# Kernel tuning notes

Hardware: AMD Instinct MI355X
Metric: run time of the kernel (lower is better)

## Reference

```python
import jax, jax.numpy as jnp
import numpy as np
import math

DIM = 256
PATCH = 16  # Patchnum
H = W = 64  # feature_size
B = 16


def _conv(x, w, pad):
    # x: [B,C,H,W], w: [O,I,kh,kw]
    return jax.lax.conv_general_dilated(
        x, w, window_strides=(1, 1), padding=[(pad, pad), (pad, pad)],
        dimension_numbers=('NCHW', 'OIHW', 'NCHW'))


def setup_inputs() -> dict:
    key = jax.random.key(0)
    ks = jax.random.split(key, 6)
    fan = DIM * 9
    s3 = 1.0 / math.sqrt(fan)
    s1 = 1.0 / math.sqrt(DIM)
    return {
        'e': jax.random.normal(ks[0], (B, DIM, H, W), dtype=jnp.float32),
        'pam_out': jax.random.normal(ks[1], (B, DIM, PATCH, PATCH), dtype=jnp.float32),
        'q_w': jax.random.uniform(ks[2], (DIM, DIM, 3, 3), jnp.float32, -s3, s3),
        'k_w': jax.random.uniform(ks[3], (DIM, DIM, 3, 3), jnp.float32, -s3, s3),
        'v_w': jax.random.uniform(ks[4], (DIM, DIM, 3, 3), jnp.float32, -s3, s3),
        'proj_w': jax.random.uniform(ks[5], (DIM, DIM, 1, 1), jnp.float32, -s1, s1),
    }


def reference(e, pam_out, q_w, k_w, v_w, proj_w):
    b, c, h, w = e.shape
    # AdaptiveAvgPool2d((PATCH, PATCH)) with h % PATCH == 0 -> mean pooling
    fh, fw = h // PATCH, w // PATCH
    max_e = e.reshape(b, c, PATCH, fh, PATCH, fw).mean(axis=(3, 5))
    q = _conv(max_e, q_w, 1).reshape(b, c, PATCH * PATCH)      # [b,c,P^2]
    k = _conv(pam_out, k_w, 1).reshape(b, c, PATCH * PATCH)    # [b,c,P^2]
    v = _conv(e, v_w, 1).reshape(b, c, h * w)                  # [b,c,HW]
    # L2 normalize along token dim (torch F.normalize, eps=1e-12)
    q = q / jnp.maximum(jnp.linalg.norm(q, axis=-1, keepdims=True), 1e-12)
    k = k / jnp.maximum(jnp.linalg.norm(k, axis=-1, keepdims=True), 1e-12)
    attn = jnp.einsum('bcn,bdn->bcd', q, k) / math.sqrt(c)     # [b,c,c]
    attn = jax.nn.softmax(attn, axis=-1)
    out = jnp.einsum('bcd,bdn->bcn', attn, v).reshape(b, c, h, w)
    out = _conv(out, proj_w, 0) + e
    return out
```

## Files before the change

kernel.cpp:

```cpp
#include <hip/hip_runtime.h>
#include <hip/hip_bf16.h>

#define NB 16
#define NC 256
#define NPIX 4096

typedef __attribute__((ext_vector_type(8))) short short8;
typedef __attribute__((ext_vector_type(4))) short short4v;
typedef __attribute__((ext_vector_type(4))) float f32x4;

static __device__ __forceinline__ ushort f2bf(float f) {
    __hip_bfloat16 h = __float2bfloat16(f);
    return *(ushort*)&h;
}

static __device__ __forceinline__ void gload_lds16(const ushort* g, ushort* l) {
    __builtin_amdgcn_global_load_lds(
        (const __attribute__((address_space(1))) unsigned int*)g,
        (__attribute__((address_space(3))) unsigned int*)l, 16, 0, 0);
}

__global__ void __launch_bounds__(256) prep_k(
    const float* __restrict__ e, const float* __restrict__ pam,
    const float* __restrict__ qw, const float* __restrict__ kw,
    const float* __restrict__ vw, const float* __restrict__ pw,
    ushort* __restrict__ maxeT, ushort* __restrict__ pamT,
    ushort* __restrict__ wqT, ushort* __restrict__ wkT,
    ushort* __restrict__ pbf, ushort* __restrict__ vwT,
    float* __restrict__ qnorm, float* __restrict__ knorm) {
    __shared__ float smem[9216];
    int blk = blockIdx.x, t = threadIdx.x;
    if (blk < 1024) {
        int b = blk >> 6, c0 = (blk & 63) * 4;
        int py = t >> 4, px4 = (t & 15) * 4;
        float s[4];
#pragma unroll
        for (int cc = 0; cc < 4; ++cc) {
            const float* p = e + (size_t)(b * 256 + c0 + cc) * NPIX;
            float a = 0.f;
#pragma unroll
            for (int r = 0; r < 4; ++r) {
                float4 v = *(const float4*)(p + (py * 4 + r) * 64 + px4);
                a += v.x + v.y + v.z + v.w;
            }
            s[cc] = a * 0.0625f;
        }
        short4v v;
#pragma unroll
        for (int cc = 0; cc < 4; ++cc) v[cc] = (short)f2bf(s[cc]);
        *(short4v*)(maxeT + (size_t)b * 65536 + (size_t)t * 256 + c0) = v;
    } else if (blk < 1280) {
        int bb = blk - 1024;
        int b = bb >> 4, cg = bb & 15;
        float (*lt)[256] = (float(*)[256])smem;
#pragma unroll
        for (int cc = 0; cc < 16; ++cc)
            lt[cc][t] = pam[(size_t)(b * 256 + cg * 16 + cc) * 256 + t];
        __syncthreads();
        ushort* dstb = pamT + (size_t)b * 65536 + (size_t)t * 256 + cg * 16;
#pragma unroll
        for (int g = 0; g < 2; ++g) {
            short8 v;
#pragma unroll
            for (int k = 0; k < 8; ++k) v[k] = (short)f2bf(lt[g * 8 + k][t]);
            *(short8*)(dstb + g * 8) = v;
        }
    } else if (blk < 1792) {
        int idx = blk - 1280;
        const float* src = (idx < 256) ? qw : kw;
        ushort* dst = (idx < 256) ? wqT : wkT;
        int o = idx & 255;
        float wv[9];
#pragma unroll
        for (int j = 0; j < 9; ++j) wv[j] = src[(size_t)o * 2304 + t * 9 + j];
#pragma unroll
        for (int j = 0; j < 9; ++j) dst[(size_t)j * 65536 + (size_t)o * 256 + t] = f2bf(wv[j]);
    } else if (blk < 1808) {
        int base = (blk - 1792) * 4096;
        for (int g = 0; g < 16; ++g) {
            int idx = base + g * 256 + t;
            pbf[idx] = f2bf(pw[idx]);
        }
    } else if (blk < 1872) {
        int d0 = (blk - 1808) * 4;
        float* lt = smem;
        for (int u = 0; u < 36; ++u) lt[u * 256 + t] = vw[(size_t)d0 * 2304 + u * 256 + t];
        __syncthreads();
#pragma unroll
        for (int r = 0; r < 9; ++r) {
            int idx = r * 256 + t;
            int i = idx / 9, j = idx % 9;
            short4v v;
#pragma unroll
            for (int dd = 0; dd < 4; ++dd) v[dd] = (short)f2bf(lt[dd * 2304 + idx]);
            *(short4v*)(vwT + ((size_t)(j * 256 + i)) * 256 + d0) = v;
        }
    } else {
        for (int g = 0; g < 16; ++g) {
            qnorm[g * 256 + t] = 0.f;
            knorm[g * 256 + t] = 0.f;
        }
    }
}

__global__ void __launch_bounds__(256, 2) conv16_mfma(const ushort* __restrict__ maxeT,
                                                      const ushort* __restrict__ pamT,
                                                      const ushort* __restrict__ wqT,
                                                      const ushort* __restrict__ wkT,
                                                      ushort* __restrict__ qb,
                                                      ushort* __restrict__ kTb,
                                                      float* __restrict__ qnorm,
                                                      float* __restrict__ knorm) {
    int blk = blockIdx.x;
    int qk = blk >> 8;
    int b  = (blk >> 4) & 15;
    int og = (blk >> 2) & 3;
    int tg = blk & 3;
    const ushort* inT = qk ? pamT : maxeT;
    const ushort* wt  = qk ? wkT : wqT;
    ushort* outp      = qk ? kTb : qb;
    float* nrm        = qk ? knorm : qnorm;
    int tid = threadIdx.x, wid = tid >> 6, lane = tid & 63;
    int wm = wid >> 1, wn = wid & 1;
    int kq = lane >> 4, l16 = lane & 15;
    int ty0 = tg * 4;
    __shared__ ushort Bs[96][256];
    __shared__ ushort As[2][64][64];
    const ushort* itb = inT + (size_t)b * 65536;
    {
#pragma unroll
        for (int j = 0; j < 12; ++j) {
            int d = (j * 4 + wid) * 64 + lane;
            int tok = d >> 5, u = d & 31;
            int lr = tok >> 4, tx = tok & 15;
            int gy = min(max(ty0 - 1 + lr, 0), 15);
            gload_lds16(itb + (gy * 16 + tx) * 256 + ((u ^ (tok & 7)) * 8),
                        &Bs[0][0] + (size_t)(j * 4 + wid) * 512);
        }
    }
    int aoff[2];
#pragma unroll
    for (int j = 0; j < 2; ++j) {
        int d = (j * 4 + wid) * 64 + lane;
        int o = d >> 3, u = d & 7;
        aoff[j] = (og * 64 + o) * 256 + ((u ^ (o & 7)) * 8);
    }
    auto stageA = [&](int s, int buf) {
        const ushort* base = wt + (size_t)(s >> 2) * 65536 + (s & 3) * 64;
#pragma unroll
        for (int j = 0; j < 2; ++j)
            gload_lds16(base + aoff[j], &As[buf][0][0] + (size_t)(j * 4 + wid) * 512);
    };
    stageA(0, 0);
    stageA(1, 1);
    __syncthreads();
    f32x4 acc[2][2];
#pragma unroll
    for (int mf = 0; mf < 2; ++mf)
#pragma unroll
        for (int nf = 0; nf < 2; ++nf) acc[mf][nf] = (f32x4){0.f, 0.f, 0.f, 0.f};
    const short8 zf = {};
    for (int s = 0; s < 36; ++s) {
        int tap = s >> 2, kh = s & 3;
        int dy = tap / 3 - 1, dx = tap % 3 - 1;
        const ushort* bp[2]; bool ok[2]; int lt7[2];
#pragma unroll
        for (int nf = 0; nf < 2; ++nf) {
            int n = tg * 64 + wn * 32 + nf * 16 + l16;
            int ny = (n >> 4) + dy, nx = (n & 15) + dx;
            ok[nf] = ((unsigned)ny < 16u) && ((unsigned)nx < 16u);
            int lrc = min(max(ny - ty0 + 1, 0), 5);
            int nxc = min(max(nx, 0), 15);
            int ltok = lrc * 16 + nxc;
            bp[nf] = &Bs[ltok][0];
            lt7[nf] = ltok & 7;
        }
#pragma unroll
        for (int kc = 0; kc < 2; ++kc) {
            int ua = kc * 4 + kq;
            int ub = kh * 8 + kc * 4 + kq;
            short8 af[2], bfr[2];
#pragma unroll
            for (int mf = 0; mf < 2; ++mf) {
                int o = wm * 32 + mf * 16 + l16;
                af[mf] = *(const short8*)(&As[s & 1][o][(ua ^ (o & 7)) * 8]);
            }
#pragma unroll
            for (int nf = 0; nf < 2; ++nf) {
                short8 v = *(const short8*)(bp[nf] + ((ub ^ lt7[nf]) * 8));
                bfr[nf] = ok[nf] ? v : zf;
            }
#pragma unroll
            for (int mf = 0; mf < 2; ++mf)
#pragma unroll
                for (int nf = 0; nf < 2; ++nf)
                    acc[mf][nf] = __builtin_amdgcn_mfma_f32_16x16x32_bf16(af[mf], bfr[nf], acc[mf][nf], 0, 0, 0);
        }
        __syncthreads();
        if (s + 2 < 36) stageA(s + 2, s & 1);
    }
    float ss[2][4];
#pragma unroll
    for (int mf = 0; mf < 2; ++mf)
#pragma unroll
        for (int r = 0; r < 4; ++r) ss[mf][r] = 0.f;
#pragma unroll
    for (int mf = 0; mf < 2; ++mf)
#pragma unroll
        for (int nf = 0; nf < 2; ++nf)
#pragma unroll
            for (int r = 0; r < 4; ++r) ss[mf][r] += acc[mf][nf][r] * acc[mf][nf][r];
#pragma unroll
    for (int mf = 0; mf < 2; ++mf)
#pragma unroll
        for (int r = 0; r < 4; ++r) {
#pragma unroll
            for (int off = 1; off < 16; off <<= 1) ss[mf][r] += __shfl_xor(ss[mf][r], off, 64);
        }
    if (l16 == 0) {
#pragma unroll
        for (int mf = 0; mf < 2; ++mf)
#pragma unroll
            for (int r = 0; r < 4; ++r)
                atomicAdd(&nrm[b * 256 + og * 64 + wm * 32 + mf * 16 + kq * 4 + r], ss[mf][r]);
    }
    ushort* ob = outp + (size_t)b * 65536;
#pragma unroll
    for (int mf = 0; mf < 2; ++mf)
#pragma unroll
        for (int nf = 0; nf < 2; ++nf) {
            int col = tg * 64 + wn * 32 + nf * 16 + l16;
#pragma unroll
            for (int r = 0; r < 4; ++r) {
                int row = og * 64 + wm * 32 + mf * 16 + kq * 4 + r;
                ob[(size_t)row * 256 + col] = f2bf(acc[mf][nf][r]);
            }
        }
}

__global__ void __launch_bounds__(512) attn_mfma(const ushort* __restrict__ qb,
                                                 const ushort* __restrict__ kTb,
                                                 const float* __restrict__ qnorm,
                                                 const float* __restrict__ knorm,
                                                 ushort* __restrict__ attnT) {
    int blk = blockIdx.x;
    int b = (blk & 7) + 8 * ((blk >> 3) & 1);
    int cg = blk >> 4;
    int tid = threadIdx.x, wid = tid >> 6, lane = tid & 63;
    int rw = wid & 3, chf = wid >> 2;
    int kq = lane >> 4, l16 = lane & 15;
    int c0w = cg * 64 + rw * 16;
    int lrow = rw * 16 + kq * 4;
    f32x4 acc[8];
#pragma unroll
    for (int nf = 0; nf < 8; ++nf) acc[nf] = (f32x4){0.f, 0.f, 0.f, 0.f};
    const ushort* qp = qb + (size_t)b * 65536;
    const ushort* kp = kTb + (size_t)b * 65536 + (size_t)(chf * 128) * 256;
    for (int kc = 0; kc < 8; ++kc) {
        short8 af = *(const short8*)(qp + (size_t)(c0w + l16) * 256 + kc * 32 + kq * 8);
#pragma unroll
        for (int nf = 0; nf < 8; ++nf) {
            short8 bf = *(const short8*)(kp + (size_t)(nf * 16 + l16) * 256 + kc * 32 + kq * 8);
            acc[nf] = __builtin_amdgcn_mfma_f32_16x16x32_bf16(af, bf, acc[nf], 0, 0, 0);
        }
    }
    float rq[4], rk[8];
#pragma unroll
    for (int r = 0; r < 4; ++r)
        rq[r] = rsqrtf(fmaxf(qnorm[b * 256 + c0w + kq * 4 + r], 1e-24f)) * 0.0625f;
#pragma unroll
    for (int nf = 0; nf < 8; ++nf)
        rk[nf] = rsqrtf(fmaxf(knorm[b * 256 + chf * 128 + nf * 16 + l16], 1e-24f));
#pragma unroll
    for (int nf = 0; nf < 8; ++nf)
#pragma unroll
        for (int r = 0; r < 4; ++r) acc[nf][r] *= rq[r] * rk[nf];
    __shared__ float red[64][2];
    float m4[4], s4[4];
#pragma unroll
    for (int r = 0; r < 4; ++r) {
        float m = -1e30f;
#pragma unroll
        for (int nf = 0; nf < 8; ++nf) m = fmaxf(m, acc[nf][r]);
#pragma unroll
        for (int off = 1; off < 16; off <<= 1) m = fmaxf(m, __shfl_xor(m, off, 64));
        m4[r] = m;
    }
    if (l16 == 0) {
#pragma unroll
        for (int r = 0; r < 4; ++r) red[lrow + r][chf] = m4[r];
    }
    __syncthreads();
#pragma unroll
    for (int r = 0; r < 4; ++r) m4[r] = fmaxf(red[lrow + r][0], red[lrow + r][1]);
    __syncthreads();
#pragma unroll
    for (int r = 0; r < 4; ++r) {
        float s = 0.f;
#pragma unroll
        for (int nf = 0; nf < 8; ++nf) {
            float ex = __expf(acc[nf][r] - m4[r]);
            acc[nf][r] = ex;
            s += ex;
        }
#pragma unroll
        for (int off = 1; off < 16; off <<= 1) s += __shfl_xor(s, off, 64);
        s4[r] = s;
    }
    if (l16 == 0) {
#pragma unroll
        for (int r = 0; r < 4; ++r) red[lrow + r][chf] = s4[r];
    }
    __syncthreads();
#pragma unroll
    for (int r = 0; r < 4; ++r) {
        float inv = 1.0f / (red[lrow + r][0] + red[lrow + r][1]);
#pragma unroll
        for (int nf = 0; nf < 8; ++nf) acc[nf][r] *= inv;
    }
    ushort* ap = attnT + (size_t)b * 65536;
#pragma unroll
    for (int nf = 0; nf < 8; ++nf) {
        int d = chf * 128 + nf * 16 + l16;
        short4v v;
#pragma unroll
        for (int r = 0; r < 4; ++r) v[r] = (short)f2bf(acc[nf][r]);
        *(short4v*)(ap + (size_t)d * 256 + c0w + kq * 4) = v;
    }
}

__global__ void __launch_bounds__(512) mproj_mfma(const ushort* __restrict__ pbf,
                                                  const ushort* __restrict__ attnT,
                                                  ushort* __restrict__ Mbf) {
    int blk = blockIdx.x;
    int b = (blk & 7) + 8 * ((blk >> 3) & 1);
    int og = blk >> 4;
    int tid = threadIdx.x, wid = tid >> 6, lane = tid & 63;
    int rw = wid & 3, chf = wid >> 2;
    int kq = lane >> 4, l16 = lane & 15;
    int o0w = og * 64 + rw * 16;
    f32x4 acc[8];
#pragma unroll
    for (int nf = 0; nf < 8; ++nf) acc[nf] = (f32x4){0.f, 0.f, 0.f, 0.f};
    const ushort* ap = attnT + (size_t)b * 65536 + (size_t)(chf * 128) * 256;
    for (int kc = 0; kc < 8; ++kc) {
        short8 af = *(const short8*)(pbf + (size_t)(o0w + l16) * 256 + kc * 32 + kq * 8);
#pragma unroll
        for (int nf = 0; nf < 8; ++nf) {
            short8 bf = *(const short8*)(ap + (size_t)(nf * 16 + l16) * 256 + kc * 32 + kq * 8);
            acc[nf] = __builtin_amdgcn_mfma_f32_16x16x32_bf16(af, bf, acc[nf], 0, 0, 0);
        }
    }
    ushort* mb = Mbf + (size_t)b * 65536;
#pragma unroll
    for (int nf = 0; nf < 8; ++nf)
#pragma unroll
        for (int r = 0; r < 4; ++r)
            mb[(size_t)(o0w + kq * 4 + r) * 256 + chf * 128 + nf * 16 + l16] = f2bf(acc[nf][r]);
}

__global__ void __launch_bounds__(512) weff_mfma(const ushort* __restrict__ Mbf,
                                                 const ushort* __restrict__ vwT,
                                                 ushort* __restrict__ wbf) {
    int blk = blockIdx.x;
    int i = blk >> 3;
    int b = (blk & 7) + 8 * (i >> 4);
    int j = i & 15;
    if (j >= 9) return;
    int tid = threadIdx.x;
    int wid = tid >> 6, lane = tid & 63;
    int wm = wid >> 1, wn = wid & 1;
    int kq = lane >> 4, l16 = lane & 15;
    f32x4 acc[4][8];
#pragma unroll
    for (int mf = 0; mf < 4; ++mf)
#pragma unroll
        for (int nf = 0; nf < 8; ++nf) acc[mf][nf] = (f32x4){0.f, 0.f, 0.f, 0.f};
    const ushort* abase = Mbf + (size_t)b * 65536 + (size_t)(wm * 64 + l16) * 256 + kq * 8;
    const ushort* bbase = vwT + (size_t)(j * 256 + wn * 128 + l16) * 256 + kq * 8;
    for (int kc = 0; kc < 8; ++kc) {
        int d0 = kc * 32;
        short8 af[4], bfr[8];
#pragma unroll
        for (int mf = 0; mf < 4; ++mf) af[mf] = *(const short8*)(abase + mf * 16 * 256 + d0);
#pragma unroll
        for (int nf = 0; nf < 8; ++nf) bfr[nf] = *(const short8*)(bbase + nf * 16 * 256 + d0);
#pragma unroll
        for (int mf = 0; mf < 4; ++mf)
#pragma unroll
            for (int nf = 0; nf < 8; ++nf)
                acc[mf][nf] = __builtin_amdgcn_mfma_f32_16x16x32_bf16(af[mf], bfr[nf], acc[mf][nf], 0, 0, 0);
    }
    ushort* wout = wbf + ((size_t)(b * 9 + j)) * 65536;
#pragma unroll
    for (int mf = 0; mf < 4; ++mf) {
        int o = wm * 64 + mf * 16 + kq * 4;
#pragma unroll
        for (int nf = 0; nf < 8; ++nf) {
            int ic = wn * 128 + nf * 16 + l16;
#pragma unroll
            for (int r = 0; r < 4; ++r)
                wout[(size_t)(o + r) * 256 + ic] = f2bf(acc[mf][nf][r]);
        }
    }
}

__global__ void __launch_bounds__(512, 4) bigconv_mfma(const float* __restrict__ e,
                                                       const ushort* __restrict__ wbf,
                                                       float* __restrict__ out) {
    int blk = blockIdx.x;
    int ibf = blk >> 3;
    int b = (blk & 7) + 8 * (ibf >> 5);
    int rem = ibf & 31;
    int pt = rem >> 1, oh = rem & 1;
    int y0 = pt * 4;
    int tid = threadIdx.x, wid = tid >> 6, lane = tid & 63;
    int wr = wid >> 1, wo = wid & 1;
    int kq = lane >> 4, l16 = lane & 15;
    __shared__ ushort Bs[6][64][64];
    __shared__ ushort As[2][128][64];
    f32x4 acc[4][4];
#pragma unroll
    for (int mf = 0; mf < 4; ++mf)
#pragma unroll
        for (int nf = 0; nf < 4; ++nf) acc[mf][nf] = (f32x4){0.f, 0.f, 0.f, 0.f};
    const float* eb = e + (size_t)b * NC * NPIX;
    const ushort* wb = wbf + (size_t)b * 589824;
    const short8 zf = {};
    int c2 = tid & 31, rr = tid >> 5;
    int sr = rr >> 1, sq = rr & 1;
    bool bstage = (rr < 12);
    int syc = min(max(y0 - 1 + sr, 0), 63);
    int ao[2], asd[2];
#pragma unroll
    for (int j = 0; j < 2; ++j) {
        int du = (j * 8 + wid) * 64 + lane;
        ao[j] = du >> 3;
        asd[j] = (lane & 7) ^ (ao[j] & 7);
    }

    for (int ci = 0; ci < 4; ++ci) {
        __syncthreads();
        if (bstage) {
            const float* s0 = eb + ((size_t)(ci * 64 + 2 * c2) * 64 + syc) * 64 + sq * 32;
            const float* s1 = s0 + NPIX;
            uint* bsrow = (uint*)&Bs[sr][0][0];
#pragma unroll
            for (int h = 0; h < 2; ++h) {
                float4 va[4], vb[4];
#pragma unroll
                for (int q = 0; q < 4; ++q) va[q] = *(const float4*)(s0 + h * 16 + q * 4);
#pragma unroll
                for (int q = 0; q < 4; ++q) vb[q] = *(const float4*)(s1 + h * 16 + q * 4);
#pragma unroll
                for (int q = 0; q < 4; ++q) {
#pragma unroll
                    for (int m2 = 0; m2 < 4; ++m2) {
                        int px = sq * 32 + h * 16 + q * 4 + m2;
                        float f0 = ((const float*)&va[q])[m2];
                        float f1 = ((const float*)&vb[q])[m2];
                        uint pk = (uint)f2bf(f0) | ((uint)f2bf(f1) << 16);
                        int s = (c2 >> 2) ^ (px & 7);
                        bsrow[px * 32 + s * 4 + (c2 & 3)] = pk;
                    }
                }
            }
        }
        {
#pragma unroll
            for (int j = 0; j < 2; ++j) {
                const ushort* src = wb + (size_t)(oh * 128 + ao[j]) * 256 + ci * 64 + asd[j] * 8;
                gload_lds16(src, &As[0][0][0] + (size_t)(j * 8 + wid) * 512);
            }
        }
        __syncthreads();
        int cur = 0;
        for (int tap = 0; tap < 9; ++tap) {
            if (tap < 8) {
#pragma unroll
                for (int j = 0; j < 2; ++j) {
                    const ushort* src = wb + (size_t)(tap + 1) * 65536 +
                                        (size_t)(oh * 128 + ao[j]) * 256 + ci * 64 + asd[j] * 8;
                    gload_lds16(src, &As[cur ^ 1][0][0] + (size_t)(j * 8 + wid) * 512);
                }
            }
            {
                int dy = tap / 3 - 1, dx = tap % 3 - 1;
                int rl = wr + dy + 1;
                bool rowok = (unsigned)(y0 + wr + dy) < 64u;
                const ushort* bp[4]; bool ok[4]; int p7[4];
#pragma unroll
                for (int nf = 0; nf < 4; ++nf) {
                    int pxr = nf * 16 + l16 + dx;
                    ok[nf] = rowok && ((unsigned)pxr < 64u);
                    int pxc = min(max(pxr, 0), 63);
                    bp[nf] = &Bs[rl][pxc][0];
                    p7[nf] = pxc & 7;
                }
#pragma unroll
                for (int kc = 0; kc < 2; ++kc) {
                    int sd = kc * 4 + kq;
                    short8 af[4];
#pragma unroll
                    for (int mf = 0; mf < 4; ++mf) {
                        int o = wo * 64 + mf * 16 + l16;
                        af[mf] = *(const short8*)(&As[cur][o][(sd ^ (o & 7)) * 8]);
                    }
                    short8 bfr[4];
#pragma unroll
                    for (int nf = 0; nf < 4; ++nf) {
                        short8 v = *(const short8*)(bp[nf] + (sd ^ p7[nf]) * 8);
                        bfr[nf] = ok[nf] ? v : zf;
                    }
#pragma unroll
                    for (int mf = 0; mf < 4; ++mf)
#pragma unroll
                        for (int nf = 0; nf < 4; ++nf)
                            acc[mf][nf] = __builtin_amdgcn_mfma_f32_16x16x32_bf16(af[mf], bfr[nf], acc[mf][nf], 0, 0, 0);
                }
            }
            __syncthreads();
            cur ^= 1;
        }
    }
    int prow = y0 + wr;
    float* ob = out + (size_t)b * NC * NPIX;
#pragma unroll
    for (int mf = 0; mf < 4; ++mf) {
        int o = oh * 128 + wo * 64 + mf * 16 + kq * 4;
#pragma unroll
        for (int nf = 0; nf < 4; ++nf) {
            int p = prow * 64 + nf * 16 + l16;
#pragma unroll
            for (int r = 0; r < 4; ++r) {
                size_t idx = (size_t)(o + r) * NPIX + p;
                ob[idx] = acc[mf][nf][r] + eb[idx];
            }
        }
    }
}

extern "C" void kernel_launch(void* const* d_in, const int* in_sizes, int n_in,
                              void* d_out, int out_size, void* d_ws, size_t ws_size,
                              hipStream_t stream) {
    const float* e   = (const float*)d_in[0];
    const float* pam = (const float*)d_in[1];
    const float* qw  = (const float*)d_in[2];
    const float* kw  = (const float*)d_in[3];
    const float* vw  = (const float*)d_in[4];
    const float* pw  = (const float*)d_in[5];
    float* out = (float*)d_out;
    float* ws  = (float*)d_ws;

    ushort* wbf  = (ushort*)ws;
    float*  S    = ws + 4718592;
    ushort* maxeT = (ushort*)S;
    ushort* pamT  = (ushort*)(S + 524288);
    ushort* wqT   = (ushort*)(S + 1048576);
    ushort* wkT   = (ushort*)(S + 1343488);
    ushort* pbf   = (ushort*)(S + 1638400);
    ushort* vwT   = (ushort*)(S + 1671168);
    float*  qnorm = S + 1966080;
    float*  knorm = S + 1970176;
    ushort* qb    = (ushort*)ws;
    ushort* kTb   = (ushort*)(ws + 524288);
    ushort* attnT = maxeT;
    ushort* Mbf   = pamT;

    prep_k<<<1873, 256, 0, stream>>>(e, pam, qw, kw, vw, pw,
                                     maxeT, pamT, wqT, wkT, pbf, vwT, qnorm, knorm);
    conv16_mfma<<<512, 256, 0, stream>>>(maxeT, pamT, wqT, wkT, qb, kTb, qnorm, knorm);
    attn_mfma<<<64, 512, 0, stream>>>(qb, kTb, qnorm, knorm, attnT);
    mproj_mfma<<<64, 512, 0, stream>>>(pbf, attnT, Mbf);
    weff_mfma<<<256, 512, 0, stream>>>(Mbf, vwT, wbf);
    bigconv_mfma<<<512, 512, 0, stream>>>(e, wbf, out);
}
```

Baseline: 204.4 us.

## Pre-transpose e to bf16 channel-last, retile attention kernels, add MFMA priority

The prep kernel now also writes a bf16, channel-last copy of e while computing the pooled tokens. Bigconv then stages its B tiles with direct global-to-LDS loads from that copy instead of converting fp32 to bf16 on every pass. attn and mproj are split into 32-row groups to launch twice as many blocks. weff skips its idle blocks by launching only the 144 it needs, and bigconv raises wave priority around its MFMA bursts. In exchange there is an extra 32 MB workspace write and read of the transposed e, and a larger workspace footprint.

New measurement: 180.7 us. -11.6%, faster.

```diff
diff --git a/kernel.cpp b/kernel.cpp
--- a/kernel.cpp
+++ b/kernel.cpp
@@ -24,33 +24,53 @@
     const float* __restrict__ e, const float* __restrict__ pam,
     const float* __restrict__ qw, const float* __restrict__ kw,
     const float* __restrict__ vw, const float* __restrict__ pw,
-    ushort* __restrict__ maxeT, ushort* __restrict__ pamT,
+    ushort* __restrict__ et, ushort* __restrict__ maxeT, ushort* __restrict__ pamT,
     ushort* __restrict__ wqT, ushort* __restrict__ wkT,
     ushort* __restrict__ pbf, ushort* __restrict__ vwT,
     float* __restrict__ qnorm, float* __restrict__ knorm) {
-    __shared__ float smem[9216];
+    __shared__ float smem[16384];
     int blk = blockIdx.x, t = threadIdx.x;
-    if (blk < 1024) {
-        int b = blk >> 6, c0 = (blk & 63) * 4;
-        int py = t >> 4, px4 = (t & 15) * 4;
-        float s[4];
-#pragma unroll
-        for (int cc = 0; cc < 4; ++cc) {
-            const float* p = e + (size_t)(b * 256 + c0 + cc) * NPIX;
-            float a = 0.f;
-#pragma unroll
-            for (int r = 0; r < 4; ++r) {
-                float4 v = *(const float4*)(p + (py * 4 + r) * 64 + px4);
-                a += v.x + v.y + v.z + v.w;
-            }
-            s[cc] = a * 0.0625f;
-        }
-        short4v v;
-#pragma unroll
-        for (int cc = 0; cc < 4; ++cc) v[cc] = (short)f2bf(s[cc]);
-        *(short4v*)(maxeT + (size_t)b * 65536 + (size_t)t * 256 + c0) = v;
-    } else if (blk < 1280) {
-        int bb = blk - 1024;
+    if (blk < 256) {
+        int b = blk >> 4, py = blk & 15;
+        float (*lt)[64] = (float(*)[64])smem;
+        float pool[16];
+#pragma unroll
+        for (int rr = 0; rr < 16; ++rr) pool[rr] = 0.f;
+        int x4 = (t & 15) * 4;
+        int cg = t >> 4;
+        for (int r = 0; r < 4; ++r) {
+            int y = py * 4 + r;
+            if (r) __syncthreads();
+            const float* ep = e + (size_t)b * NC * NPIX + y * 64;
+#pragma unroll
+            for (int rr = 0; rr < 16; ++rr) {
+                int c = rr * 16 + cg;
+                float4 v = *(const float4*)(ep + (size_t)c * NPIX + x4);
+                pool[rr] += v.x + v.y + v.z + v.w;
+                int s = (c >> 3) & 31;
+                lt[c][(x4 + 0) ^ s] = v.x;
+                lt[c][(x4 + 1) ^ s] = v.y;
+                lt[c][(x4 + 2) ^ s] = v.z;
+                lt[c][(x4 + 3) ^ s] = v.w;
+            }
+            __syncthreads();
+            int l = t & 31, c0 = l * 8;
+            ushort* op = et + ((size_t)(b * 64 + y) * 64) * 256;
+            for (int rx = 0; rx < 8; ++rx) {
+                int x = rx * 8 + (t >> 5);
+                short8 v;
+#pragma unroll
+                for (int k = 0; k < 8; ++k) v[k] = (short)f2bf(lt[c0 + k][x ^ l]);
+                *(short8*)(op + (size_t)x * 256 + c0) = v;
+            }
+        }
+        int tok = py * 16 + (t & 15);
+        ushort* md = maxeT + (size_t)b * 65536 + (size_t)tok * 256;
+#pragma unroll
+        for (int rr = 0; rr < 16; ++rr)
+            md[rr * 16 + cg] = f2bf(pool[rr] * 0.0625f);
+    } else if (blk < 512) {
+        int bb = blk - 256;
         int b = bb >> 4, cg = bb & 15;
         float (*lt)[256] = (float(*)[256])smem;
 #pragma unroll
@@ -65,8 +85,8 @@
             for (int k = 0; k < 8; ++k) v[k] = (short)f2bf(lt[g * 8 + k][t]);
             *(short8*)(dstb + g * 8) = v;
         }
-    } else if (blk < 1792) {
-        int idx = blk - 1280;
+    } else if (blk < 1024) {
+        int idx = blk - 512;
         const float* src = (idx < 256) ? qw : kw;
         ushort* dst = (idx < 256) ? wqT : wkT;
         int o = idx & 255;
@@ -75,14 +95,14 @@
         for (int j = 0; j < 9; ++j) wv[j] = src[(size_t)o * 2304 + t * 9 + j];
 #pragma unroll
         for (int j = 0; j < 9; ++j) dst[(size_t)j * 65536 + (size_t)o * 256 + t] = f2bf(wv[j]);
-    } else if (blk < 1808) {
-        int base = (blk - 1792) * 4096;
+    } else if (blk < 1040) {
+        int base = (blk - 1024) * 4096;
         for (int g = 0; g < 16; ++g) {
             int idx = base + g * 256 + t;
             pbf[idx] = f2bf(pw[idx]);
         }
-    } else if (blk < 1872) {
-        int d0 = (blk - 1808) * 4;
+    } else if (blk < 1104) {
+        int d0 = (blk - 1040) * 4;
         float* lt = smem;
         for (int u = 0; u < 36; ++u) lt[u * 256 + t] = vw[(size_t)d0 * 2304 + u * 256 + t];
         __syncthreads();
@@ -247,41 +267,41 @@
     int b = (blk & 7) + 8 * ((blk >> 3) & 1);
     int cg = blk >> 4;
     int tid = threadIdx.x, wid = tid >> 6, lane = tid & 63;
-    int rw = wid & 3, chf = wid >> 2;
+    int rw = wid & 1, chf = wid >> 1;
     int kq = lane >> 4, l16 = lane & 15;
-    int c0w = cg * 64 + rw * 16;
+    int c0w = cg * 32 + rw * 16;
     int lrow = rw * 16 + kq * 4;
-    f32x4 acc[8];
-#pragma unroll
-    for (int nf = 0; nf < 8; ++nf) acc[nf] = (f32x4){0.f, 0.f, 0.f, 0.f};
+    f32x4 acc[4];
+#pragma unroll
+    for (int nf = 0; nf < 4; ++nf) acc[nf] = (f32x4){0.f, 0.f, 0.f, 0.f};
     const ushort* qp = qb + (size_t)b * 65536;
-    const ushort* kp = kTb + (size_t)b * 65536 + (size_t)(chf * 128) * 256;
+    const ushort* kp = kTb + (size_t)b * 65536 + (size_t)(chf * 64) * 256;
     for (int kc = 0; kc < 8; ++kc) {
         short8 af = *(const short8*)(qp + (size_t)(c0w + l16) * 256 + kc * 32 + kq * 8);
 #pragma unroll
-        for (int nf = 0; nf < 8; ++nf) {
+        for (int nf = 0; nf < 4; ++nf) {
             short8 bf = *(const short8*)(kp + (size_t)(nf * 16 + l16) * 256 + kc * 32 + kq * 8);
             acc[nf] = __builtin_amdgcn_mfma_f32_16x16x32_bf16(af, bf, acc[nf], 0, 0, 0);
         }
     }
-    float rq[4], rk[8];
+    float rq[4], rk[4];
 #pragma unroll
     for (int r = 0; r < 4; ++r)
         rq[r] = rsqrtf(fmaxf(qnorm[b * 256 + c0w + kq * 4 + r], 1e-24f)) * 0.0625f;
 #pragma unroll
-    for (int nf = 0; nf < 8; ++nf)
-        rk[nf] = rsqrtf(fmaxf(knorm[b * 256 + chf * 128 + nf * 16 + l16], 1e-24f));
-#pragma unroll
-    for (int nf = 0; nf < 8; ++nf)
+    for (int nf = 0; nf < 4; ++nf)
+        rk[nf] = rsqrtf(fmaxf(knorm[b * 256 + chf * 64 + nf * 16 + l16], 1e-24f));
+#pragma unroll
+    for (int nf = 0; nf < 4; ++nf)
 #pragma unroll
         for (int r = 0; r < 4; ++r) acc[nf][r] *= rq[r] * rk[nf];
-    __shared__ float red[64][2];
+    __shared__ float red[32][4];
     float m4[4], s4[4];
 #pragma unroll
     for (int r = 0; r < 4; ++r) {
         float m = -1e30f;
 #pragma unroll
-        for (int nf = 0; nf < 8; ++nf) m = fmaxf(m, acc[nf][r]);
+        for (int nf = 0; nf < 4; ++nf) m = fmaxf(m, acc[nf][r]);
 #pragma unroll
         for (int off = 1; off < 16; off <<= 1) m = fmaxf(m, __shfl_xor(m, off, 64));
         m4[r] = m;
@@ -292,13 +312,15 @@
     }
     __syncthreads();
 #pragma unroll
-    for (int r = 0; r < 4; ++r) m4[r] = fmaxf(red[lrow + r][0], red[lrow + r][1]);
+    for (int r = 0; r < 4; ++r)
+        m4[r] = fmaxf(fmaxf(red[lrow + r][0], red[lrow + r][1]),
+                      fmaxf(red[lrow + r][2], red[lrow + r][3]));
     __syncthreads();
 #pragma unroll
     for (int r = 0; r < 4; ++r) {
         float s = 0.f;
 #pragma unroll
-        for (int nf = 0; nf < 8; ++nf) {
+        for (int nf = 0; nf < 4; ++nf) {
             float ex = __expf(acc[nf][r] - m4[r]);
             acc[nf][r] = ex;
             s += ex;
@@ -314,14 +336,15 @@
     __syncthreads();
 #pragma unroll
     for (int r = 0; r < 4; ++r) {
-        float inv = 1.0f / (red[lrow + r][0] + red[lrow + r][1]);
-#pragma unroll
-        for (int nf = 0; nf < 8; ++nf) acc[nf][r] *= inv;
+        float inv = 1.0f / (red[lrow + r][0] + red[lrow + r][1] +
+                            red[lrow + r][2] + red[lrow + r][3]);
+#pragma unroll
+        for (int nf = 0; nf < 4; ++nf) acc[nf][r] *= inv;
     }
     ushort* ap = attnT + (size_t)b * 65536;
 #pragma unroll
-    for (int nf = 0; nf < 8; ++nf) {
-        int d = chf * 128 + nf * 16 + l16;
+    for (int nf = 0; nf < 4; ++nf) {
+        int d = chf * 64 + nf * 16 + l16;
         short4v v;
 #pragma unroll
         for (int r = 0; r < 4; ++r) v[r] = (short)f2bf(acc[nf][r]);
@@ -336,37 +359,35 @@
     int b = (blk & 7) + 8 * ((blk >> 3) & 1);
     int og = blk >> 4;
     int tid = threadIdx.x, wid = tid >> 6, lane = tid & 63;
-    int rw = wid & 3, chf = wid >> 2;
+    int rw = wid & 1, chf = wid >> 1;
     int kq = lane >> 4, l16 = lane & 15;
-    int o0w = og * 64 + rw * 16;
-    f32x4 acc[8];
-#pragma unroll
-    for (int nf = 0; nf < 8; ++nf) acc[nf] = (f32x4){0.f, 0.f, 0.f, 0.f};
-    const ushort* ap = attnT + (size_t)b * 65536 + (size_t)(chf * 128) * 256;
+    int o0w = og * 32 + rw * 16;
+    f32x4 acc[4];
+#pragma unroll
+    for (int nf = 0; nf < 4; ++nf) acc[nf] = (f32x4){0.f, 0.f, 0.f, 0.f};
+    const ushort* ap = attnT + (size_t)b * 65536 + (size_t)(chf * 64) * 256;
     for (int kc = 0; kc < 8; ++kc) {
         short8 af = *(const short8*)(pbf + (size_t)(o0w + l16) * 256 + kc * 32 + kq * 8);
 #pragma unroll
-        for (int nf = 0; nf < 8; ++nf) {
+        for (int nf = 0; nf < 4; ++nf) {
             short8 bf = *(const short8*)(ap + (size_t)(nf * 16 + l16) * 256 + kc * 32 + kq * 8);
             acc[nf] = __builtin_amdgcn_mfma_f32_16x16x32_bf16(af, bf, acc[nf], 0, 0, 0);
         }
     }
     ushort* mb = Mbf + (size_t)b * 65536;
 #pragma unroll
-    for (int nf = 0; nf < 8; ++nf)
+    for (int nf = 0; nf < 4; ++nf)
 #pragma unroll
         for (int r = 0; r < 4; ++r)
-            mb[(size_t)(o0w + kq * 4 + r) * 256 + chf * 128 + nf * 16 + l16] = f2bf(acc[nf][r]);
+            mb[(size_t)(o0w + kq * 4 + r) * 256 + chf * 64 + nf * 16 + l16] = f2bf(acc[nf][r]);
 }
 
 __global__ void __launch_bounds__(512) weff_mfma(const ushort* __restrict__ Mbf,
                                                  const ushort* __restrict__ vwT,
                                                  ushort* __restrict__ wbf) {
     int blk = blockIdx.x;
-    int i = blk >> 3;
-    int b = (blk & 7) + 8 * (i >> 4);
-    int j = i & 15;
-    if (j >= 9) return;
+    int wg = (blk % 8) * 18 + blk / 8;
+    int b = wg / 9, j = wg % 9;
     int tid = threadIdx.x;
     int wid = tid >> 6, lane = tid & 63;
     int wm = wid >> 1, wn = wid & 1;
@@ -405,8 +426,9 @@
     }
 }
 
-__global__ void __launch_bounds__(512, 4) bigconv_mfma(const float* __restrict__ e,
+__global__ void __launch_bounds__(512, 4) bigconv_mfma(const ushort* __restrict__ et,
                                                        const ushort* __restrict__ wbf,
+                                                       const float* __restrict__ e,
                                                        float* __restrict__ out) {
     int blk = blockIdx.x;
     int ibf = blk >> 3;
@@ -424,66 +446,43 @@
     for (int mf = 0; mf < 4; ++mf)
 #pragma unroll
         for (int nf = 0; nf < 4; ++nf) acc[mf][nf] = (f32x4){0.f, 0.f, 0.f, 0.f};
+    const ushort* etb = et + (size_t)b * 1048576;
     const float* eb = e + (size_t)b * NC * NPIX;
     const ushort* wb = wbf + (size_t)b * 589824;
     const short8 zf = {};
-    int c2 = tid & 31, rr = tid >> 5;
-    int sr = rr >> 1, sq = rr & 1;
-    bool bstage = (rr < 12);
-    int syc = min(max(y0 - 1 + sr, 0), 63);
+    int bpx = (tid >> 3) & 63, bu = tid & 7;
+    int bsw = (bu ^ (bpx & 7)) * 8;
+    int byc[6];
+#pragma unroll
+    for (int j = 0; j < 6; ++j) byc[j] = min(max(y0 - 1 + j, 0), 63);
     int ao[2], asd[2];
 #pragma unroll
     for (int j = 0; j < 2; ++j) {
         int du = (j * 8 + wid) * 64 + lane;
         ao[j] = du >> 3;
-        asd[j] = (lane & 7) ^ (ao[j] & 7);
-    }
+        asd[j] = (du & 7) ^ (ao[j] & 7);
+    }
+    auto stageA = [&](int tap, int buf, int ci) {
+        const ushort* base = wb + (size_t)tap * 65536 + ci * 64;
+#pragma unroll
+        for (int j = 0; j < 2; ++j)
+            gload_lds16(base + (size_t)(oh * 128 + ao[j]) * 256 + asd[j] * 8,
+                        &As[buf][0][0] + (size_t)(j * 8 + wid) * 512);
+    };
 
     for (int ci = 0; ci < 4; ++ci) {
+        {
+#pragma unroll
+            for (int j = 0; j < 6; ++j) {
+                const ushort* src = etb + (((size_t)(byc[j] * 64 + bpx)) << 8) + ci * 64 + bsw;
+                gload_lds16(src, &Bs[0][0][0] + (size_t)(j * 4096 + wid * 512));
+            }
+        }
+        stageA(0, 0, ci);
         __syncthreads();
-        if (bstage) {
-            const float* s0 = eb + ((size_t)(ci * 64 + 2 * c2) * 64 + syc) * 64 + sq * 32;
-            const float* s1 = s0 + NPIX;
-            uint* bsrow = (uint*)&Bs[sr][0][0];
-#pragma unroll
-            for (int h = 0; h < 2; ++h) {
-                float4 va[4], vb[4];
-#pragma unroll
-                for (int q = 0; q < 4; ++q) va[q] = *(const float4*)(s0 + h * 16 + q * 4);
-#pragma unroll
-                for (int q = 0; q < 4; ++q) vb[q] = *(const float4*)(s1 + h * 16 + q * 4);
-#pragma unroll
-                for (int q = 0; q < 4; ++q) {
-#pragma unroll
-                    for (int m2 = 0; m2 < 4; ++m2) {
-                        int px = sq * 32 + h * 16 + q * 4 + m2;
-                        float f0 = ((const float*)&va[q])[m2];
-                        float f1 = ((const float*)&vb[q])[m2];
-                        uint pk = (uint)f2bf(f0) | ((uint)f2bf(f1) << 16);
-                        int s = (c2 >> 2) ^ (px & 7);
-                        bsrow[px * 32 + s * 4 + (c2 & 3)] = pk;
-                    }
-                }
-            }
-        }
-        {
-#pragma unroll
-            for (int j = 0; j < 2; ++j) {
-                const ushort* src = wb + (size_t)(oh * 128 + ao[j]) * 256 + ci * 64 + asd[j] * 8;
-                gload_lds16(src, &As[0][0][0] + (size_t)(j * 8 + wid) * 512);
-            }
-        }
-        __syncthreads();
-        int cur = 0;
         for (int tap = 0; tap < 9; ++tap) {
-            if (tap < 8) {
-#pragma unroll
-                for (int j = 0; j < 2; ++j) {
-                    const ushort* src = wb + (size_t)(tap + 1) * 65536 +
-                                        (size_t)(oh * 128 + ao[j]) * 256 + ci * 64 + asd[j] * 8;
-                    gload_lds16(src, &As[cur ^ 1][0][0] + (size_t)(j * 8 + wid) * 512);
-                }
-            }
+            int cur = tap & 1;
+            if (tap < 8) stageA(tap + 1, cur ^ 1, ci);
             {
                 int dy = tap / 3 - 1, dx = tap % 3 - 1;
                 int rl = wr + dy + 1;
@@ -512,15 +511,16 @@
                         short8 v = *(const short8*)(bp[nf] + (sd ^ p7[nf]) * 8);
                         bfr[nf] = ok[nf] ? v : zf;
                     }
+                    __builtin_amdgcn_s_setprio(1);
 #pragma unroll
                     for (int mf = 0; mf < 4; ++mf)
 #pragma unroll
                         for (int nf = 0; nf < 4; ++nf)
                             acc[mf][nf] = __builtin_amdgcn_mfma_f32_16x16x32_bf16(af[mf], bfr[nf], acc[mf][nf], 0, 0, 0);
+                    __builtin_amdgcn_s_setprio(0);
                 }
             }
             __syncthreads();
-            cur ^= 1;
         }
     }
     int prow = y0 + wr;
@@ -552,8 +552,9 @@
     float* out = (float*)d_out;
     float* ws  = (float*)d_ws;
 
-    ushort* wbf  = (ushort*)ws;
-    float*  S    = ws + 4718592;
+    ushort* et   = (ushort*)ws;
+    ushort* wbf  = (ushort*)(ws + 8388608);
+    float*  S    = ws + 13107200;
     ushort* maxeT = (ushort*)S;
     ushort* pamT  = (ushort*)(S + 524288);
     ushort* wqT   = (ushort*)(S + 1048576);
@@ -562,16 +563,16 @@
     ushort* vwT   = (ushort*)(S + 1671168);
     float*  qnorm = S + 1966080;
     float*  knorm = S + 1970176;
-    ushort* qb    = (ushort*)ws;
-    ushort* kTb   = (ushort*)(ws + 524288);
+    ushort* qb    = (ushort*)(ws + 8388608);
+    ushort* kTb   = (ushort*)(ws + 8912896);
     ushort* attnT = maxeT;
     ushort* Mbf   = pamT;
 
-    prep_k<<<1873, 256, 0, stream>>>(e, pam, qw, kw, vw, pw,
-                                     maxeT, pamT, wqT, wkT, pbf, vwT, qnorm, knorm);
+    prep_k<<<1105, 256, 0, stream>>>(e, pam, qw, kw, vw, pw,
+                                     et, maxeT, pamT, wqT, wkT, pbf, vwT, qnorm, knorm);
     conv16_mfma<<<512, 256, 0, stream>>>(maxeT, pamT, wqT, wkT, qb, kTb, qnorm, knorm);
-    attn_mfma<<<64, 512, 0, stream>>>(qb, kTb, qnorm, knorm, attnT);
-    mproj_mfma<<<64, 512, 0, stream>>>(pbf, attnT, Mbf);
-    weff_mfma<<<256, 512, 0, stream>>>(Mbf, vwT, wbf);
-    bigconv_mfma<<<512, 512, 0, stream>>>(e, wbf, out);
-}
+    attn_mfma<<<128, 512, 0, stream>>>(qb, kTb, qnorm, knorm, attnT);
+    mproj_mfma<<<128, 512, 0, stream>>>(pbf, attnT, Mbf);
+    weff_mfma<<<144, 512, 0, stream>>>(Mbf, vwT, wbf);
+    bigconv_mfma<<<512, 512, 0, stream>>>(et, wbf, e, out);
+}
```
